# Kernel tuning notes

Measured on AMD Instinct MI355X. Metric: run time of the kernel, lower is better.

## Reference

```python
import jax, jax.numpy as jnp
import numpy as np

B, IN, H = 8192, 2048, 2048
EFF = IN + H  # self_recurrent concat of [x_t, state]


def setup_inputs() -> dict:
    key = jax.random.key(0)
    ks = jax.random.split(key, 6)
    s_in = 1.0 / np.sqrt(EFF).astype(np.float32)
    s_h = 1.0 / np.sqrt(H).astype(np.float32)
    return {
        "x_t": jax.random.normal(ks[0], (B, IN), jnp.float32),
        "state": jax.random.normal(ks[1], (B, H), jnp.float32),
        "Wc": jax.random.normal(ks[2], (EFF, H), jnp.float32) * s_in,
        "Uc": jax.random.normal(ks[3], (H, H), jnp.float32) * s_h,
        "bc": jnp.zeros((H,), jnp.float32),
        "Wg": jax.random.normal(ks[4], (EFF, H), jnp.float32) * s_in,
        "Ug": jax.random.normal(ks[5], (H, H), jnp.float32) * s_h,
        "bg": jnp.zeros((H,), jnp.float32),
        "log_step": jnp.zeros((H,), jnp.float32),  # dt_scale=1.0 -> no init shift
        "gamma": jnp.ones((H,), jnp.float32),
        "beta": jnp.zeros((H,), jnp.float32),
    }


def _layernorm(x, gamma, beta, eps=1e-5):
    mu = jnp.mean(x, axis=-1, keepdims=True)
    var = jnp.mean((x - mu) ** 2, axis=-1, keepdims=True)
    return (x - mu) * jax.lax.rsqrt(var + eps) * gamma + beta


def reference(x_t, state, Wc, Uc, bc, Wg, Ug, bg, log_step, gamma, beta):
    dt = 1.0  # step(dt=1.0) * dt_scale(1.0)
    xin = jnp.concatenate([x_t, state], axis=-1)        # [B, EFF], self_recurrent
    cand = jnp.tanh(xin @ Wc + state @ Uc + bc)          # candidate state [B, H]
    gate = jax.nn.sigmoid(xin @ Wg + state @ Ug + bg)    # input gate [B, H]
    tau = jnp.exp(log_step)                              # learned time constant
    alpha = jnp.exp(-dt / tau)                           # exp(-dt/tau) decay
    h_new = alpha * state + (1.0 - alpha) * gate * cand  # liquid gated update
    return _layernorm(h_new, gamma, beta)                # post-norm
```

## Files before the change

### kernel.cpp

```cpp
#include <hip/hip_runtime.h>
#include <hip/hip_bf16.h>
#include <cstdint>
#include <cstddef>

#define Bsz 8192
#define Hdim 2048
#define Kdim 4096
#define Nall 4096

#define BM 256
#define BNH 128
#define BK 64
#define NTILES (Kdim / BK)
#define NITER (NTILES / 2)

typedef __attribute__((ext_vector_type(8))) short short8;
typedef __attribute__((ext_vector_type(4))) short short4v;
typedef __attribute__((ext_vector_type(4))) float floatx4;

__device__ __forceinline__ short f2bf(float f) {
    unsigned u = __float_as_uint(f);
    unsigned r = (u + 0x7fffu + ((u >> 16) & 1u)) >> 16;
    return (short)(r & 0xffffu);
}

__device__ __forceinline__ float fast_tanh(float x) {
    float e = __expf(2.f * x);
    return 1.f - 2.f / (e + 1.f);
}
__device__ __forceinline__ float fast_sigmoid(float x) {
    return 1.f / (1.f + __expf(-x));
}

__device__ __forceinline__ void g2l16(const void* g, void* l) {
    __builtin_amdgcn_global_load_lds(
        (const __attribute__((address_space(1))) unsigned int*)g,
        (__attribute__((address_space(3))) unsigned int*)l,
        16, 0, 0);
}

__global__ __launch_bounds__(256) void build_wt(
    const float* __restrict__ Wc, const float* __restrict__ Uc,
    const float* __restrict__ Wg, const float* __restrict__ Ug,
    short* __restrict__ Wt)
{
    __shared__ float tile[64][257];
    const int nt = blockIdx.x * 64;
    const int kt = blockIdx.y * 256;
    const int tx = threadIdx.x & 15;
    const int ty = threadIdx.x >> 4;

    const bool isGate = (nt >= Hdim);
    const float* W = isGate ? Wg : Wc;
    const float* U = isGate ? Ug : Uc;
    const int ncol = isGate ? (nt - Hdim) : nt;
    const bool useU = (kt >= Hdim);

#pragma unroll 4
    for (int r = 0; r < 256; r += 16) {
        int k = kt + ty + r;
        float4 v = *(const float4*)(W + (size_t)k * Hdim + ncol + tx * 4);
        if (useU) {
            float4 u = *(const float4*)(U + (size_t)(k - Hdim) * Hdim + ncol + tx * 4);
            v.x += u.x; v.y += u.y; v.z += u.z; v.w += u.w;
        }
        int kl = ty + r;
        tile[tx * 4 + 0][kl] = v.x;
        tile[tx * 4 + 1][kl] = v.y;
        tile[tx * 4 + 2][kl] = v.z;
        tile[tx * 4 + 3][kl] = v.w;
    }
    __syncthreads();

    const int n  = threadIdx.x >> 2;
    const int kq = (threadIdx.x & 3) * 64;
    short* dst = Wt + (size_t)(nt + n) * Kdim + kt + kq;
#pragma unroll
    for (int i = 0; i < 8; ++i) {
        short8 o;
#pragma unroll
        for (int e = 0; e < 8; ++e) o[e] = f2bf(tile[n][kq + i * 8 + e]);
        *(short8*)(dst + i * 8) = o;
    }
}

__global__ __launch_bounds__(256) void build_acat(
    const float* __restrict__ x, const float* __restrict__ st,
    short* __restrict__ A)
{
    const int lane = threadIdx.x & 63;
    const int wid = (blockIdx.x * 256 + threadIdx.x) >> 6;
    const size_t base = (size_t)wid * 512;
    const int row = (int)(base >> 12);
    const int c = (int)(base & 4095);
    const float* src = (c < Hdim) ? (x + (size_t)row * Hdim + c)
                                  : (st + (size_t)row * Hdim + (c - Hdim));
    float4 v0 = *(const float4*)(src + lane * 4);
    float4 v1 = *(const float4*)(src + 256 + lane * 4);
    short4v o0, o1;
    o0[0] = f2bf(v0.x); o0[1] = f2bf(v0.y); o0[2] = f2bf(v0.z); o0[3] = f2bf(v0.w);
    o1[0] = f2bf(v1.x); o1[1] = f2bf(v1.y); o1[2] = f2bf(v1.z); o1[3] = f2bf(v1.w);
    short* d = A + base;
    *(short4v*)(d + lane * 4) = o0;
    *(short4v*)(d + 256 + lane * 4) = o1;
}

__device__ __forceinline__ void rdA4(const short* base, const int i0,
                                     short8 (&aF)[4][2],
                                     const int cs0, const int cs1) {
#pragma unroll
    for (int i = 0; i < 4; ++i) {
        aF[i][0] = *(const short8*)(base + (i0 + i) * 16 * BK + cs0);
        aF[i][1] = *(const short8*)(base + (i0 + i) * 16 * BK + cs1);
    }
}
__device__ __forceinline__ void rdB2(const short* base, const int j0,
                                     short8 (&bF)[2][2],
                                     const int cs0, const int cs1) {
#pragma unroll
    for (int j = 0; j < 2; ++j) {
        bF[j][0] = *(const short8*)(base + (j0 + j) * 16 * BK + cs0);
        bF[j][1] = *(const short8*)(base + (j0 + j) * 16 * BK + cs1);
    }
}
__device__ __forceinline__ void mma16(floatx4 (&acc)[8][4], const int ia,
                                      const int jb, const short8 (&aF)[4][2],
                                      const short8 (&bF)[2][2]) {
#pragma unroll
    for (int i = 0; i < 4; ++i)
#pragma unroll
        for (int j = 0; j < 2; ++j) {
            acc[ia + i][jb + j] = __builtin_amdgcn_mfma_f32_16x16x32_bf16(
                aF[i][0], bF[j][0], acc[ia + i][jb + j], 0, 0, 0);
            acc[ia + i][jb + j] = __builtin_amdgcn_mfma_f32_16x16x32_bf16(
                aF[i][1], bF[j][1], acc[ia + i][jb + j], 0, 0, 0);
        }
}

#define STAGE(srcArr, h, dstBase, dstOff, koff) do {               \
    g2l16(srcArr[h][0] + (koff), (dstBase) + dstOff[h][0]);        \
    g2l16(srcArr[h][1] + (koff), (dstBase) + dstOff[h][1]); } while (0)

#define BAR()   __builtin_amdgcn_s_barrier()
#define LGKM0() asm volatile("s_waitcnt lgkmcnt(0)" ::: "memory")
#define VM6()   asm volatile("s_waitcnt vmcnt(6)" ::: "memory")
#define VM0()   asm volatile("s_waitcnt vmcnt(0)" ::: "memory")
#define PRIO1() __builtin_amdgcn_s_setprio(1)
#define PRIO0() __builtin_amdgcn_s_setprio(0)

__global__ __launch_bounds__(512, 2) void gemm_fused(
    const short* __restrict__ A,
    const short* __restrict__ Bt,
    const float* __restrict__ st,
    const float* __restrict__ bc, const float* __restrict__ bg,
    const float* __restrict__ lstep,
    float* __restrict__ Hout)
{
    __shared__ __attribute__((aligned(16))) short lds[4][256 * BK];
    short* const sA0 = &lds[0][0];
    short* const sA1 = &lds[1][0];
    short* const sB0 = &lds[2][0];
    short* const sB1 = &lds[3][0];

    const int tid  = threadIdx.x;
    const int lane = tid & 63;
    const int w    = tid >> 6;
    const int wm   = w >> 2;
    const int wn   = w & 3;

    const int bid = blockIdx.x;
    const int swz = (bid & 7) * 64 + (bid >> 3);
    const int m0 = (swz >> 4) * BM;
    const int n0 = (swz & 15) * BNH;

    const int r8 = lane >> 3;
    const int c8 = ((lane & 7) ^ r8) * 8;
    const short* aSrc[2][2];
    const short* bSrc[2][2];
    int dstA[2][2], dstB[2][2];
#pragma unroll
    for (int h = 0; h < 2; ++h)
#pragma unroll
        for (int q = 0; q < 2; ++q) {
            int f = w * 2 + q;
            int ra = f * 8 + h * 64 + (f & 8) * 8;
            int rb = (f >> 2) * 64 + (f & 3) * 8 + h * 32;
            aSrc[h][q] = A + (size_t)(m0 + ra + r8) * Kdim + c8;
            int lr = rb + r8;
            int btrow = n0 + ((lr >> 6) << 5) + (lr & 31)
                        + ((lr & 32) ? Hdim : 0);
            bSrc[h][q] = Bt + (size_t)btrow * Kdim + c8;
            dstA[h][q] = ra * BK;
            dstB[h][q] = rb * BK;
        }

    const int fr = lane & 15;
    const int j4 = lane >> 4;
    const int cs0 = ((j4 ^ (fr & 7)) * 8);
    const int cs1 = (((4 + j4) ^ (fr & 7)) * 8);
    const short* A0f = sA0 + (wm * 128 + fr) * BK;
    const short* A1f = sA1 + (wm * 128 + fr) * BK;
    const short* B0f = sB0 + (wn * 64 + fr) * BK;
    const short* B1f = sB1 + (wn * 64 + fr) * BK;

    floatx4 acc[8][4];
#pragma unroll
    for (int i = 0; i < 8; ++i)
#pragma unroll
        for (int j = 0; j < 4; ++j) {
            floatx4 z = {0.f, 0.f, 0.f, 0.f};
            acc[i][j] = z;
        }
    short8 aF[4][2], bLo[2][2], bHi[2][2];

    STAGE(aSrc, 0, sA0, dstA, 0);
    STAGE(aSrc, 1, sA0, dstA, 0);
    STAGE(bSrc, 0, sB0, dstB, 0);
    STAGE(bSrc, 1, sB0, dstB, 0);
    STAGE(aSrc, 0, sA1, dstA, BK);
    STAGE(bSrc, 0, sB1, dstB, BK);
    STAGE(bSrc, 1, sB1, dstB, BK);
    VM6();
    BAR();

    for (int it = 0; it < NITER; ++it) {
        const bool nl = (it < NITER - 1);
        const int k1  = (2 * it + 1) * BK;
        const int k02 = (2 * it + 2) * BK;
        const int k12 = (2 * it + 3) * BK;

        rdA4(A0f, 0, aF, cs0, cs1);
        rdB2(B0f, 0, bLo, cs0, cs1);
        STAGE(aSrc, 1, sA1, dstA, k1);
        BAR(); LGKM0(); PRIO1();
        mma16(acc, 0, 0, aF, bLo);
        PRIO0(); BAR();

        rdB2(B0f, 2, bHi, cs0, cs1);
        if (nl) { STAGE(aSrc, 0, sA0, dstA, k02); }
        BAR(); LGKM0(); PRIO1();
        mma16(acc, 0, 2, aF, bHi);
        PRIO0(); BAR();

        rdA4(A0f, 4, aF, cs0, cs1);
        if (nl) { STAGE(bSrc, 0, sB0, dstB, k02); }
        BAR(); LGKM0(); PRIO1();
        mma16(acc, 4, 0, aF, bLo);
        PRIO0(); BAR();

        if (nl) { STAGE(bSrc, 1, sB0, dstB, k02); VM6(); }
        else    { VM0(); }
        BAR(); PRIO1();
        mma16(acc, 4, 2, aF, bHi);
        PRIO0(); BAR();

        rdA4(A1f, 0, aF, cs0, cs1);
        rdB2(B1f, 0, bLo, cs0, cs1);
        if (nl) { STAGE(aSrc, 1, sA0, dstA, k02); }
        BAR(); LGKM0(); PRIO1();
        mma16(acc, 0, 0, aF, bLo);
        PRIO0(); BAR();

        rdB2(B1f, 2, bHi, cs0, cs1);
        if (nl) { STAGE(aSrc, 0, sA1, dstA, k12); }
        BAR(); LGKM0(); PRIO1();
        mma16(acc, 0, 2, aF, bHi);
        PRIO0(); BAR();

        rdA4(A1f, 4, aF, cs0, cs1);
        if (nl) { STAGE(bSrc, 0, sB1, dstB, k12); }
        BAR(); LGKM0(); PRIO1();
        mma16(acc, 4, 0, aF, bLo);
        PRIO0(); BAR();

        if (nl) { STAGE(bSrc, 1, sB1, dstB, k12); VM6(); }
        BAR(); PRIO1();
        mma16(acc, 4, 2, aF, bHi);
        PRIO0(); BAR();
    }

    const int cn = lane & 15;
    const int cr = j4 * 4;
    float bcv[2], bgv[2], alv[2];
#pragma unroll
    for (int j = 0; j < 2; ++j) {
        int col = n0 + wn * 32 + j * 16 + cn;
        bcv[j] = bc[col];
        bgv[j] = bg[col];
        alv[j] = __expf(-__expf(-lstep[col]));
    }
#pragma unroll
    for (int i = 0; i < 8; ++i) {
        int rowb = m0 + wm * 128 + i * 16 + cr;
#pragma unroll
        for (int r = 0; r < 4; ++r) {
            int row = rowb + r;
            const float* sp = st + (size_t)row * Hdim;
            float* hp = Hout + (size_t)row * Hdim;
#pragma unroll
            for (int j = 0; j < 2; ++j) {
                int col = n0 + wn * 32 + j * 16 + cn;
                float cand = fast_tanh(acc[i][j][r] + bcv[j]);
                float gate = fast_sigmoid(acc[i][j + 2][r] + bgv[j]);
                float al = alv[j];
                hp[col] = al * sp[col] + (1.f - al) * gate * cand;
            }
        }
    }
}

__global__ __launch_bounds__(256) void ln_k(
    const float* __restrict__ h, const float* __restrict__ gam,
    const float* __restrict__ bet, float* __restrict__ out)
{
    const int lane = threadIdx.x & 63;
    const int b = blockIdx.x * 4 + (threadIdx.x >> 6);
    const float* hp = h + (size_t)b * Hdim;

    float4 v[8];
    float sum = 0.f, ss = 0.f;
#pragma unroll
    for (int i = 0; i < 8; ++i) {
        v[i] = *(const float4*)(hp + i * 256 + lane * 4);
        sum += v[i].x + v[i].y + v[i].z + v[i].w;
        ss  += v[i].x * v[i].x + v[i].y * v[i].y
             + v[i].z * v[i].z + v[i].w * v[i].w;
    }
#pragma unroll
    for (int off = 1; off < 64; off <<= 1) {
        sum += __shfl_xor(sum, off);
        ss  += __shfl_xor(ss, off);
    }

    const float inv = 1.f / (float)Hdim;
    float mu = sum * inv;
    float var = ss * inv - mu * mu;
    float rs = rsqrtf(var + 1e-5f);

    float* op = out + (size_t)b * Hdim;
#pragma unroll
    for (int i = 0; i < 8; ++i) {
        float4 g  = *(const float4*)(gam + i * 256 + lane * 4);
        float4 be = *(const float4*)(bet + i * 256 + lane * 4);
        float4 o;
        o.x = (v[i].x - mu) * rs * g.x + be.x;
        o.y = (v[i].y - mu) * rs * g.y + be.y;
        o.z = (v[i].z - mu) * rs * g.z + be.z;
        o.w = (v[i].w - mu) * rs * g.w + be.w;
        *(float4*)(op + i * 256 + lane * 4) = o;
    }
}

extern "C" void kernel_launch(void* const* d_in, const int* in_sizes, int n_in,
                              void* d_out, int out_size, void* d_ws, size_t ws_size,
                              hipStream_t stream)
{
    const float* x_t   = (const float*)d_in[0];
    const float* state = (const float*)d_in[1];
    const float* Wc    = (const float*)d_in[2];
    const float* Uc    = (const float*)d_in[3];
    const float* bc    = (const float*)d_in[4];
    const float* Wg    = (const float*)d_in[5];
    const float* Ug    = (const float*)d_in[6];
    const float* bg    = (const float*)d_in[7];
    const float* lstep = (const float*)d_in[8];
    const float* gam   = (const float*)d_in[9];
    const float* bet   = (const float*)d_in[10];
    float* out = (float*)d_out;

    char* ws = (char*)d_ws;
    short* Wt   = (short*)ws;
    short* Acat = (short*)(ws + (size_t)32 * 1024 * 1024);
    float* h    = (float*)(ws + (size_t)96 * 1024 * 1024);

    build_wt<<<dim3(Nall / 64, Kdim / 256), 256, 0, stream>>>(Wc, Uc, Wg, Ug, Wt);
    build_acat<<<(Bsz * (Kdim / 8)) / 256, 256, 0, stream>>>(x_t, state, Acat);
    gemm_fused<<<dim3((Bsz / BM) * (Hdim / BNH)), 512, 0, stream>>>(
        Acat, Wt, state, bc, bg, lstep, h);
    ln_k<<<Bsz / 4, 256, 0, stream>>>(h, gam, bet, out);
}
```

Before: 501.5 us.

## Fuse all four stages into one persistent kernel with grid-wide barriers

```diff
diff --git a/kernel.cpp b/kernel.cpp
--- a/kernel.cpp
+++ b/kernel.cpp
@@ -23,7 +23,6 @@
     unsigned r = (u + 0x7fffu + ((u >> 16) & 1u)) >> 16;
     return (short)(r & 0xffffu);
 }
-
 __device__ __forceinline__ float fast_tanh(float x) {
     float e = __expf(2.f * x);
     return 1.f - 2.f / (e + 1.f);
@@ -31,12 +30,330 @@
 __device__ __forceinline__ float fast_sigmoid(float x) {
     return 1.f / (1.f + __expf(-x));
 }
-
 __device__ __forceinline__ void g2l16(const void* g, void* l) {
     __builtin_amdgcn_global_load_lds(
         (const __attribute__((address_space(1))) unsigned int*)g,
         (__attribute__((address_space(3))) unsigned int*)l,
         16, 0, 0);
+}
+
+__device__ __forceinline__ void grid_sync(int* cnt, int target) {
+    __syncthreads();
+    if (threadIdx.x == 0) {
+        __threadfence();
+        atomicAdd(cnt, 1);
+        int guard = 0;
+        while (atomicAdd(cnt, 0) < target && guard < (1 << 17)) {
+            __builtin_amdgcn_s_sleep(2);
+            ++guard;
+        }
+        __threadfence();
+    }
+    __syncthreads();
+}
+
+__device__ __forceinline__ void rdA4(const short* base, const int i0,
+                                     short8 (&aF)[4][2],
+                                     const int cs0, const int cs1) {
+#pragma unroll
+    for (int i = 0; i < 4; ++i) {
+        aF[i][0] = *(const short8*)(base + (i0 + i) * 16 * BK + cs0);
+        aF[i][1] = *(const short8*)(base + (i0 + i) * 16 * BK + cs1);
+    }
+}
+__device__ __forceinline__ void rdB2(const short* base, const int j0,
+                                     short8 (&bF)[2][2],
+                                     const int cs0, const int cs1) {
+#pragma unroll
+    for (int j = 0; j < 2; ++j) {
+        bF[j][0] = *(const short8*)(base + (j0 + j) * 16 * BK + cs0);
+        bF[j][1] = *(const short8*)(base + (j0 + j) * 16 * BK + cs1);
+    }
+}
+__device__ __forceinline__ void mma16(floatx4 (&acc)[8][4], const int ia,
+                                      const int jb, const short8 (&aF)[4][2],
+                                      const short8 (&bF)[2][2]) {
+#pragma unroll
+    for (int i = 0; i < 4; ++i)
+#pragma unroll
+        for (int j = 0; j < 2; ++j) {
+            acc[ia + i][jb + j] = __builtin_amdgcn_mfma_f32_16x16x32_bf16(
+                aF[i][0], bF[j][0], acc[ia + i][jb + j], 0, 0, 0);
+            acc[ia + i][jb + j] = __builtin_amdgcn_mfma_f32_16x16x32_bf16(
+                aF[i][1], bF[j][1], acc[ia + i][jb + j], 0, 0, 0);
+        }
+}
+
+#define STAGE(srcArr, h, dstBase, dstOff, koff) do {               \
+    g2l16(srcArr[h][0] + (koff), (dstBase) + dstOff[h][0]);        \
+    g2l16(srcArr[h][1] + (koff), (dstBase) + dstOff[h][1]); } while (0)
+
+#define BAR()   __builtin_amdgcn_s_barrier()
+#define LGKM0() asm volatile("s_waitcnt lgkmcnt(0)" ::: "memory")
+#define VM6()   asm volatile("s_waitcnt vmcnt(6)" ::: "memory")
+#define VM0()   asm volatile("s_waitcnt vmcnt(0)" ::: "memory")
+#define PRIO1() __builtin_amdgcn_s_setprio(1)
+#define PRIO0() __builtin_amdgcn_s_setprio(0)
+
+__global__ __launch_bounds__(512, 2) void mega(
+    const float* __restrict__ x, const float* __restrict__ st,
+    const float* __restrict__ Wc, const float* __restrict__ Uc,
+    const float* __restrict__ bc, const float* __restrict__ Wg,
+    const float* __restrict__ Ug, const float* __restrict__ bg,
+    const float* __restrict__ lstep, const float* __restrict__ gam,
+    const float* __restrict__ bet,
+    short* __restrict__ Wt, short* __restrict__ Acat,
+    float* __restrict__ h, float* __restrict__ out,
+    int* __restrict__ cnt)
+{
+    __shared__ __attribute__((aligned(16))) short lds[4][256 * BK];
+    const int tid = threadIdx.x;
+    const int bid = blockIdx.x;
+    const int lane = tid & 63;
+    const int w = tid >> 6;
+
+    {
+        float (*tile)[257] = (float(*)[257])(&lds[0][0]);
+        const int txl = tid & 15;
+        const int tyl = tid >> 4;
+#pragma unroll 1
+        for (int t4 = 0; t4 < 4; ++t4) {
+            int t = bid * 4 + t4;
+            int nt = (t & 63) * 64;
+            int kt = (t >> 6) * 256;
+            const bool isGate = (nt >= Hdim);
+            const float* W = isGate ? Wg : Wc;
+            const float* U = isGate ? Ug : Uc;
+            const int ncol = isGate ? (nt - Hdim) : nt;
+            const bool useU = (kt >= Hdim);
+#pragma unroll
+            for (int r = 0; r < 256; r += 32) {
+                int k = kt + tyl + r;
+                float4 v = *(const float4*)(W + (size_t)k * Hdim + ncol + txl * 4);
+                if (useU) {
+                    float4 u = *(const float4*)(U + (size_t)(k - Hdim) * Hdim + ncol + txl * 4);
+                    v.x += u.x; v.y += u.y; v.z += u.z; v.w += u.w;
+                }
+                int kl = tyl + r;
+                tile[txl * 4 + 0][kl] = v.x;
+                tile[txl * 4 + 1][kl] = v.y;
+                tile[txl * 4 + 2][kl] = v.z;
+                tile[txl * 4 + 3][kl] = v.w;
+            }
+            __syncthreads();
+            const int n  = tid & 63;
+            const int kq = (tid >> 6) * 32;
+            short* dst = Wt + (size_t)(nt + n) * Kdim + kt + kq;
+#pragma unroll
+            for (int i = 0; i < 4; ++i) {
+                short8 o;
+#pragma unroll
+                for (int e = 0; e < 8; ++e) o[e] = f2bf(tile[n][kq + i * 8 + e]);
+                *(short8*)(dst + i * 8) = o;
+            }
+            __syncthreads();
+        }
+#pragma unroll 1
+        for (int i = 0; i < 32; ++i) {
+            int seg = bid * 8 + w + i * 2048;
+            size_t base = (size_t)seg * 512;
+            int row = (int)(base >> 12);
+            int c = (int)(base & 4095);
+            const float* src = (c < Hdim) ? (x + (size_t)row * Hdim + c)
+                                          : (st + (size_t)row * Hdim + (c - Hdim));
+            float4 v0 = *(const float4*)(src + lane * 4);
+            float4 v1 = *(const float4*)(src + 256 + lane * 4);
+            short4v o0, o1;
+            o0[0] = f2bf(v0.x); o0[1] = f2bf(v0.y); o0[2] = f2bf(v0.z); o0[3] = f2bf(v0.w);
+            o1[0] = f2bf(v1.x); o1[1] = f2bf(v1.y); o1[2] = f2bf(v1.z); o1[3] = f2bf(v1.w);
+            short* d = Acat + base;
+            *(short4v*)(d + lane * 4) = o0;
+            *(short4v*)(d + 256 + lane * 4) = o1;
+        }
+    }
+    grid_sync(cnt, 256);
+
+    {
+        short* const sA0 = &lds[0][0];
+        short* const sA1 = &lds[1][0];
+        short* const sB0 = &lds[2][0];
+        short* const sB1 = &lds[3][0];
+        const int wm = w >> 2;
+        const int wn = w & 3;
+        const int r8 = lane >> 3;
+        const int c8 = ((lane & 7) ^ r8) * 8;
+        const int fr = lane & 15;
+        const int j4 = lane >> 4;
+        const int cs0 = ((j4 ^ (fr & 7)) * 8);
+        const int cs1 = (((4 + j4) ^ (fr & 7)) * 8);
+        const short* A0f = sA0 + (wm * 128 + fr) * BK;
+        const short* A1f = sA1 + (wm * 128 + fr) * BK;
+        const short* B0f = sB0 + (wn * 64 + fr) * BK;
+        const short* B1f = sB1 + (wn * 64 + fr) * BK;
+
+#pragma unroll 1
+        for (int rep = 0; rep < 2; ++rep) {
+            const int vb = bid + rep * 256;
+            const int swz = (vb & 7) * 64 + (vb >> 3);
+            const int m0 = (swz >> 4) * BM;
+            const int n0 = (swz & 15) * BNH;
+
+            const short* aSrc[2][2];
+            const short* bSrc[2][2];
+            int dstA[2][2], dstB[2][2];
+#pragma unroll
+            for (int hh = 0; hh < 2; ++hh)
+#pragma unroll
+                for (int q = 0; q < 2; ++q) {
+                    int f = w * 2 + q;
+                    int ra = f * 8 + hh * 64 + (f & 8) * 8;
+                    int rb = (f >> 2) * 64 + (f & 3) * 8 + hh * 32;
+                    aSrc[hh][q] = Acat + (size_t)(m0 + ra + r8) * Kdim + c8;
+                    int lr = rb + r8;
+                    int btrow = n0 + ((lr >> 6) << 5) + (lr & 31)
+                                + ((lr & 32) ? Hdim : 0);
+                    bSrc[hh][q] = Wt + (size_t)btrow * Kdim + c8;
+                    dstA[hh][q] = ra * BK;
+                    dstB[hh][q] = rb * BK;
+                }
+
+            floatx4 acc[8][4];
+#pragma unroll
+            for (int i = 0; i < 8; ++i)
+#pragma unroll
+                for (int j = 0; j < 4; ++j) {
+                    floatx4 z = {0.f, 0.f, 0.f, 0.f};
+                    acc[i][j] = z;
+                }
+            short8 aF[4][2], bLo[2][2], bHi[2][2];
+
+            STAGE(aSrc, 0, sA0, dstA, 0);
+            STAGE(aSrc, 1, sA0, dstA, 0);
+            STAGE(bSrc, 0, sB0, dstB, 0);
+            STAGE(bSrc, 1, sB0, dstB, 0);
+            STAGE(aSrc, 0, sA1, dstA, BK);
+            STAGE(bSrc, 0, sB1, dstB, BK);
+            STAGE(bSrc, 1, sB1, dstB, BK);
+            VM6();
+            BAR();
+
+#pragma unroll 1
+            for (int it = 0; it < NITER; ++it) {
+                const bool nl = (it < NITER - 1);
+                const int k1  = (2 * it + 1) * BK;
+                const int k02 = (2 * it + 2) * BK;
+                const int k12 = (2 * it + 3) * BK;
+
+                rdA4(A0f, 0, aF, cs0, cs1);
+                rdB2(B0f, 0, bLo, cs0, cs1);
+                STAGE(aSrc, 1, sA1, dstA, k1);
+                BAR(); LGKM0(); PRIO1();
+                mma16(acc, 0, 0, aF, bLo);
+                PRIO0(); BAR();
+                rdB2(B0f, 2, bHi, cs0, cs1);
+                if (nl) { STAGE(aSrc, 0, sA0, dstA, k02); }
+                BAR(); LGKM0(); PRIO1();
+                mma16(acc, 0, 2, aF, bHi);
+                PRIO0(); BAR();
+                rdA4(A0f, 4, aF, cs0, cs1);
+                if (nl) { STAGE(bSrc, 0, sB0, dstB, k02); }
+                BAR(); LGKM0(); PRIO1();
+                mma16(acc, 4, 0, aF, bLo);
+                PRIO0(); BAR();
+                if (nl) { STAGE(bSrc, 1, sB0, dstB, k02); VM6(); }
+                else    { VM0(); }
+                BAR(); PRIO1();
+                mma16(acc, 4, 2, aF, bHi);
+                PRIO0(); BAR();
+                rdA4(A1f, 0, aF, cs0, cs1);
+                rdB2(B1f, 0, bLo, cs0, cs1);
+                if (nl) { STAGE(aSrc, 1, sA0, dstA, k02); }
+                BAR(); LGKM0(); PRIO1();
+                mma16(acc, 0, 0, aF, bLo);
+                PRIO0(); BAR();
+                rdB2(B1f, 2, bHi, cs0, cs1);
+                if (nl) { STAGE(aSrc, 0, sA1, dstA, k12); }
+                BAR(); LGKM0(); PRIO1();
+                mma16(acc, 0, 2, aF, bHi);
+                PRIO0(); BAR();
+                rdA4(A1f, 4, aF, cs0, cs1);
+                if (nl) { STAGE(bSrc, 0, sB1, dstB, k12); }
+                BAR(); LGKM0(); PRIO1();
+                mma16(acc, 4, 0, aF, bLo);
+                PRIO0(); BAR();
+                if (nl) { STAGE(bSrc, 1, sB1, dstB, k12); VM6(); }
+                BAR(); PRIO1();
+                mma16(acc, 4, 2, aF, bHi);
+                PRIO0(); BAR();
+            }
+
+            const int cn = lane & 15;
+            const int cr = j4 * 4;
+            float bcv[2], bgv[2], alv[2];
+#pragma unroll
+            for (int j = 0; j < 2; ++j) {
+                int col = n0 + wn * 32 + j * 16 + cn;
+                bcv[j] = bc[col];
+                bgv[j] = bg[col];
+                alv[j] = __expf(-__expf(-lstep[col]));
+            }
+#pragma unroll
+            for (int i = 0; i < 8; ++i) {
+                int rowb = m0 + wm * 128 + i * 16 + cr;
+#pragma unroll
+                for (int r = 0; r < 4; ++r) {
+                    int row = rowb + r;
+                    const float* sp = st + (size_t)row * Hdim;
+                    float* hp = h + (size_t)row * Hdim;
+#pragma unroll
+                    for (int j = 0; j < 2; ++j) {
+                        int col = n0 + wn * 32 + j * 16 + cn;
+                        float cand = fast_tanh(acc[i][j][r] + bcv[j]);
+                        float gate = fast_sigmoid(acc[i][j + 2][r] + bgv[j]);
+                        float al = alv[j];
+                        hp[col] = al * sp[col] + (1.f - al) * gate * cand;
+                    }
+                }
+            }
+        }
+    }
+    grid_sync(cnt, 512);
+
+#pragma unroll 1
+    for (int i = 0; i < 4; ++i) {
+        int b = bid * 32 + w * 4 + i;
+        const float* hp = h + (size_t)b * Hdim;
+        float4 v[8];
+        float sum = 0.f, ss = 0.f;
+#pragma unroll
+        for (int q = 0; q < 8; ++q) {
+            v[q] = *(const float4*)(hp + q * 256 + lane * 4);
+            sum += v[q].x + v[q].y + v[q].z + v[q].w;
+            ss  += v[q].x * v[q].x + v[q].y * v[q].y
+                 + v[q].z * v[q].z + v[q].w * v[q].w;
+        }
+#pragma unroll
+        for (int off = 1; off < 64; off <<= 1) {
+            sum += __shfl_xor(sum, off);
+            ss  += __shfl_xor(ss, off);
+        }
+        const float inv = 1.f / (float)Hdim;
+        float mu = sum * inv;
+        float var = ss * inv - mu * mu;
+        float rs = rsqrtf(var + 1e-5f);
+        float* op = out + (size_t)b * Hdim;
+#pragma unroll
+        for (int q = 0; q < 8; ++q) {
+            float4 g  = *(const float4*)(gam + q * 256 + lane * 4);
+            float4 be = *(const float4*)(bet + q * 256 + lane * 4);
+            float4 o;
+            o.x = (v[q].x - mu) * rs * g.x + be.x;
+            o.y = (v[q].y - mu) * rs * g.y + be.y;
+            o.z = (v[q].z - mu) * rs * g.z + be.z;
+            o.w = (v[q].w - mu) * rs * g.w + be.w;
+            *(float4*)(op + q * 256 + lane * 4) = o;
+        }
+    }
 }
 
 __global__ __launch_bounds__(256) void build_wt(
@@ -49,13 +366,11 @@
     const int kt = blockIdx.y * 256;
     const int tx = threadIdx.x & 15;
     const int ty = threadIdx.x >> 4;
-
     const bool isGate = (nt >= Hdim);
     const float* W = isGate ? Wg : Wc;
     const float* U = isGate ? Ug : Uc;
     const int ncol = isGate ? (nt - Hdim) : nt;
     const bool useU = (kt >= Hdim);
-
 #pragma unroll 4
     for (int r = 0; r < 256; r += 16) {
         int k = kt + ty + r;
@@ -71,7 +386,6 @@
         tile[tx * 4 + 3][kl] = v.w;
     }
     __syncthreads();
-
     const int n  = threadIdx.x >> 2;
     const int kq = (threadIdx.x & 3) * 64;
     short* dst = Wt + (size_t)(nt + n) * Kdim + kt + kq;
@@ -105,55 +419,10 @@
     *(short4v*)(d + 256 + lane * 4) = o1;
 }
 
-__device__ __forceinline__ void rdA4(const short* base, const int i0,
-                                     short8 (&aF)[4][2],
-                                     const int cs0, const int cs1) {
-#pragma unroll
-    for (int i = 0; i < 4; ++i) {
-        aF[i][0] = *(const short8*)(base + (i0 + i) * 16 * BK + cs0);
-        aF[i][1] = *(const short8*)(base + (i0 + i) * 16 * BK + cs1);
-    }
-}
-__device__ __forceinline__ void rdB2(const short* base, const int j0,
-                                     short8 (&bF)[2][2],
-                                     const int cs0, const int cs1) {
-#pragma unroll
-    for (int j = 0; j < 2; ++j) {
-        bF[j][0] = *(const short8*)(base + (j0 + j) * 16 * BK + cs0);
-        bF[j][1] = *(const short8*)(base + (j0 + j) * 16 * BK + cs1);
-    }
-}
-__device__ __forceinline__ void mma16(floatx4 (&acc)[8][4], const int ia,
-                                      const int jb, const short8 (&aF)[4][2],
-                                      const short8 (&bF)[2][2]) {
-#pragma unroll
-    for (int i = 0; i < 4; ++i)
-#pragma unroll
-        for (int j = 0; j < 2; ++j) {
-            acc[ia + i][jb + j] = __builtin_amdgcn_mfma_f32_16x16x32_bf16(
-                aF[i][0], bF[j][0], acc[ia + i][jb + j], 0, 0, 0);
-            acc[ia + i][jb + j] = __builtin_amdgcn_mfma_f32_16x16x32_bf16(
-                aF[i][1], bF[j][1], acc[ia + i][jb + j], 0, 0, 0);
-        }
-}
-
-#define STAGE(srcArr, h, dstBase, dstOff, koff) do {               \
-    g2l16(srcArr[h][0] + (koff), (dstBase) + dstOff[h][0]);        \
-    g2l16(srcArr[h][1] + (koff), (dstBase) + dstOff[h][1]); } while (0)
-
-#define BAR()   __builtin_amdgcn_s_barrier()
-#define LGKM0() asm volatile("s_waitcnt lgkmcnt(0)" ::: "memory")
-#define VM6()   asm volatile("s_waitcnt vmcnt(6)" ::: "memory")
-#define VM0()   asm volatile("s_waitcnt vmcnt(0)" ::: "memory")
-#define PRIO1() __builtin_amdgcn_s_setprio(1)
-#define PRIO0() __builtin_amdgcn_s_setprio(0)
-
 __global__ __launch_bounds__(512, 2) void gemm_fused(
-    const short* __restrict__ A,
-    const short* __restrict__ Bt,
-    const float* __restrict__ st,
-    const float* __restrict__ bc, const float* __restrict__ bg,
-    const float* __restrict__ lstep,
+    const short* __restrict__ A, const short* __restrict__ Bt,
+    const float* __restrict__ st, const float* __restrict__ bc,
+    const float* __restrict__ bg, const float* __restrict__ lstep,
     float* __restrict__ Hout)
 {
     __shared__ __attribute__((aligned(16))) short lds[4][256 * BK];
@@ -161,39 +430,34 @@
     short* const sA1 = &lds[1][0];
     short* const sB0 = &lds[2][0];
     short* const sB1 = &lds[3][0];
-
-    const int tid  = threadIdx.x;
+    const int tid = threadIdx.x;
     const int lane = tid & 63;
-    const int w    = tid >> 6;
-    const int wm   = w >> 2;
-    const int wn   = w & 3;
-
+    const int w = tid >> 6;
+    const int wm = w >> 2;
+    const int wn = w & 3;
     const int bid = blockIdx.x;
     const int swz = (bid & 7) * 64 + (bid >> 3);
     const int m0 = (swz >> 4) * BM;
     const int n0 = (swz & 15) * BNH;
-
     const int r8 = lane >> 3;
     const int c8 = ((lane & 7) ^ r8) * 8;
     const short* aSrc[2][2];
     const short* bSrc[2][2];
     int dstA[2][2], dstB[2][2];
 #pragma unroll
-    for (int h = 0; h < 2; ++h)
+    for (int hh = 0; hh < 2; ++hh)
 #pragma unroll
         for (int q = 0; q < 2; ++q) {
             int f = w * 2 + q;
-            int ra = f * 8 + h * 64 + (f & 8) * 8;
-            int rb = (f >> 2) * 64 + (f & 3) * 8 + h * 32;
-            aSrc[h][q] = A + (size_t)(m0 + ra + r8) * Kdim + c8;
+            int ra = f * 8 + hh * 64 + (f & 8) * 8;
+            int rb = (f >> 2) * 64 + (f & 3) * 8 + hh * 32;
+            aSrc[hh][q] = A + (size_t)(m0 + ra + r8) * Kdim + c8;
             int lr = rb + r8;
-            int btrow = n0 + ((lr >> 6) << 5) + (lr & 31)
-                        + ((lr & 32) ? Hdim : 0);
-            bSrc[h][q] = Bt + (size_t)btrow * Kdim + c8;
-            dstA[h][q] = ra * BK;
-            dstB[h][q] = rb * BK;
-        }
-
+            int btrow = n0 + ((lr >> 6) << 5) + (lr & 31) + ((lr & 32) ? Hdim : 0);
+            bSrc[hh][q] = Bt + (size_t)btrow * Kdim + c8;
+            dstA[hh][q] = ra * BK;
+            dstB[hh][q] = rb * BK;
+        }
     const int fr = lane & 15;
     const int j4 = lane >> 4;
     const int cs0 = ((j4 ^ (fr & 7)) * 8);
@@ -202,7 +466,6 @@
     const short* A1f = sA1 + (wm * 128 + fr) * BK;
     const short* B0f = sB0 + (wn * 64 + fr) * BK;
     const short* B1f = sB1 + (wn * 64 + fr) * BK;
-
     floatx4 acc[8][4];
 #pragma unroll
     for (int i = 0; i < 8; ++i)
@@ -212,7 +475,6 @@
             acc[i][j] = z;
         }
     short8 aF[4][2], bLo[2][2], bHi[2][2];
-
     STAGE(aSrc, 0, sA0, dstA, 0);
     STAGE(aSrc, 1, sA0, dstA, 0);
     STAGE(bSrc, 0, sB0, dstB, 0);
@@ -222,63 +484,53 @@
     STAGE(bSrc, 1, sB1, dstB, BK);
     VM6();
     BAR();
-
     for (int it = 0; it < NITER; ++it) {
         const bool nl = (it < NITER - 1);
         const int k1  = (2 * it + 1) * BK;
         const int k02 = (2 * it + 2) * BK;
         const int k12 = (2 * it + 3) * BK;
-
         rdA4(A0f, 0, aF, cs0, cs1);
         rdB2(B0f, 0, bLo, cs0, cs1);
         STAGE(aSrc, 1, sA1, dstA, k1);
         BAR(); LGKM0(); PRIO1();
         mma16(acc, 0, 0, aF, bLo);
         PRIO0(); BAR();
-
         rdB2(B0f, 2, bHi, cs0, cs1);
         if (nl) { STAGE(aSrc, 0, sA0, dstA, k02); }
         BAR(); LGKM0(); PRIO1();
         mma16(acc, 0, 2, aF, bHi);
         PRIO0(); BAR();
-
         rdA4(A0f, 4, aF, cs0, cs1);
         if (nl) { STAGE(bSrc, 0, sB0, dstB, k02); }
         BAR(); LGKM0(); PRIO1();
         mma16(acc, 4, 0, aF, bLo);
         PRIO0(); BAR();
-
         if (nl) { STAGE(bSrc, 1, sB0, dstB, k02); VM6(); }
         else    { VM0(); }
         BAR(); PRIO1();
         mma16(acc, 4, 2, aF, bHi);
         PRIO0(); BAR();
-
         rdA4(A1f, 0, aF, cs0, cs1);
         rdB2(B1f, 0, bLo, cs0, cs1);
         if (nl) { STAGE(aSrc, 1, sA0, dstA, k02); }
         BAR(); LGKM0(); PRIO1();
         mma16(acc, 0, 0, aF, bLo);
         PRIO0(); BAR();
-
         rdB2(B1f, 2, bHi, cs0, cs1);
         if (nl) { STAGE(aSrc, 0, sA1, dstA, k12); }
         BAR(); LGKM0(); PRIO1();
         mma16(acc, 0, 2, aF, bHi);
         PRIO0(); BAR();
-
         rdA4(A1f, 4, aF, cs0, cs1);
         if (nl) { STAGE(bSrc, 0, sB1, dstB, k12); }
         BAR(); LGKM0(); PRIO1();
         mma16(acc, 4, 0, aF, bLo);
         PRIO0(); BAR();
-
         if (nl) { STAGE(bSrc, 1, sB1, dstB, k12); VM6(); }
         BAR(); PRIO1();
         mma16(acc, 4, 2, aF, bHi);
         PRIO0(); BAR();
     }
-
     const int cn = lane & 15;
     const int cr = j4 * 4;
     float bcv[2], bgv[2], alv[2];
@@ -316,7 +568,6 @@
     const int lane = threadIdx.x & 63;
     const int b = blockIdx.x * 4 + (threadIdx.x >> 6);
     const float* hp = h + (size_t)b * Hdim;
-
     float4 v[8];
     float sum = 0.f, ss = 0.f;
 #pragma unroll
@@ -331,12 +582,10 @@
         sum += __shfl_xor(sum, off);
         ss  += __shfl_xor(ss, off);
     }
-
     const float inv = 1.f / (float)Hdim;
     float mu = sum * inv;
     float var = ss * inv - mu * mu;
     float rs = rsqrtf(var + 1e-5f);
-
     float* op = out + (size_t)b * Hdim;
 #pragma unroll
     for (int i = 0; i < 8; ++i) {
@@ -372,10 +621,17 @@
     short* Wt   = (short*)ws;
     short* Acat = (short*)(ws + (size_t)32 * 1024 * 1024);
     float* h    = (float*)(ws + (size_t)96 * 1024 * 1024);
-
-    build_wt<<<dim3(Nall / 64, Kdim / 256), 256, 0, stream>>>(Wc, Uc, Wg, Ug, Wt);
-    build_acat<<<(Bsz * (Kdim / 8)) / 256, 256, 0, stream>>>(x_t, state, Acat);
-    gemm_fused<<<dim3((Bsz / BM) * (Hdim / BNH)), 512, 0, stream>>>(
-        Acat, Wt, state, bc, bg, lstep, h);
-    ln_k<<<Bsz / 4, 256, 0, stream>>>(h, gam, bet, out);
-}
+    int*   cnt  = (int*)(ws + (size_t)160 * 1024 * 1024);
+
+    if (ws_size >= (size_t)160 * 1024 * 1024 + 64) {
+        hipMemsetAsync(cnt, 0, 64, stream);
+        mega<<<256, 512, 0, stream>>>(x_t, state, Wc, Uc, bc, Wg, Ug, bg,
+                                      lstep, gam, bet, Wt, Acat, h, out, cnt);
+    } else {
+        build_wt<<<dim3(Nall / 64, Kdim / 256), 256, 0, stream>>>(Wc, Uc, Wg, Ug, Wt);
+        build_acat<<<(Bsz * (Kdim / 8)) / 256, 256, 0, stream>>>(x_t, state, Acat);
+        gemm_fused<<<dim3((Bsz / BM) * (Hdim / BNH)), 512, 0, stream>>>(
+            Acat, Wt, state, bc, bg, lstep, h);
+        ln_k<<<Bsz / 4, 256, 0, stream>>>(h, gam, bet, out);
+    }
+}
```

Result: slower. 555.5 us (+10.8%).
